# Performance work log

Measured on AMD Instinct MI355X. Metric: run time of the kernel, lower is better.

The kernel has to match this reference:

```python
import jax, jax.numpy as jnp
import numpy as np

B, S, E, H = 2, 2048, 1024, 16
D = E // H  # head_dim = 64
EPS = 1e-6


def _angle_decay():
    # angle: 1/10000**linspace(0,1,D//2), each value repeated twice (interleaved)
    a = 1.0 / (10000.0 ** jnp.linspace(0.0, 1.0, D // 2))
    angle = jnp.repeat(a, 2)  # [D]
    decay = jnp.log(1.0 - 2.0 ** (-5.0 - jnp.arange(H, dtype=jnp.float32)))  # [H]
    return angle, decay


def _rel_pos(slen):
    angle, decay = _angle_decay()
    idx = jnp.arange(slen, dtype=jnp.float32)
    sin = jnp.sin(idx[:, None] * angle[None, :])  # [S, D]
    cos = jnp.cos(idx[:, None] * angle[None, :])  # [S, D]
    diff = idx[:, None] - idx[None, :]            # [S, S]
    tril = diff >= 0
    masked = jnp.where(tril, diff, jnp.inf)
    mask = jnp.exp(masked * decay[:, None, None])  # [H, S, S]; exp(-inf)=0 on upper tri
    mask = jnp.nan_to_num(mask)
    mask = mask / jnp.sqrt(jnp.sum(mask, axis=-1, keepdims=True))
    return sin, cos, mask


def _rotate_every_two(x):
    x1 = x[..., ::2]
    x2 = x[..., 1::2]
    return jnp.stack((-x2, x1), axis=-1).reshape(x.shape)


def _theta_shift(x, sin, cos):
    # x: [B, H, S, D]; sin/cos: [S, D] broadcast over B,H
    return x * cos + _rotate_every_two(x) * sin


def setup_inputs() -> dict:
    key = jax.random.key(0)
    ks = jax.random.split(key, 5)
    scale = 1.0 / np.sqrt(E)
    return {
        "x": jax.random.normal(ks[0], (B, S, E), dtype=jnp.float32),
        "Wq": jax.random.normal(ks[1], (E, E), dtype=jnp.float32) * scale,
        "Wk": jax.random.normal(ks[2], (E, E), dtype=jnp.float32) * scale,
        "Wv": jax.random.normal(ks[3], (E, E), dtype=jnp.float32) * scale,
        "Wg": jax.random.normal(ks[4], (E, E), dtype=jnp.float32) * scale,
    }


def reference(x, Wq, Wk, Wv, Wg):
    bsz, tgt_len, _ = x.shape
    sin, cos, mask = _rel_pos(tgt_len)
    scaling = E ** (-0.5)

    q = x @ Wq
    k = (x @ Wk) * scaling
    v = x @ Wv
    g = x @ Wg

    q = q.reshape(bsz, tgt_len, H, D).transpose(0, 2, 1, 3)  # [B,H,S,D]
    k = k.reshape(bsz, tgt_len, H, D).transpose(0, 2, 1, 3)
    vr = v.reshape(bsz, tgt_len, H, D).transpose(0, 2, 1, 3)

    qr = _theta_shift(q, sin, cos)
    kr = _theta_shift(k, sin, cos)

    qk = jnp.einsum("bhqd,bhkd->bhqk", qr, kr) * mask[None]
    denom = jax.lax.stop_gradient(
        jnp.clip(jnp.sum(jnp.abs(qk), axis=-1, keepdims=True), 1.0, 5e4)
    )
    out = jnp.einsum("bhqk,bhkd->bhqd", qk / denom, vr)
    out = out.transpose(0, 2, 1, 3)  # [B,S,H,D]

    # RMSNorm over head_dim (no affine)
    out = out * jax.lax.rsqrt(jnp.mean(out * out, axis=-1, keepdims=True) + EPS)
    out = out.reshape(bsz, tgt_len, E)
    return jax.nn.silu(g) * out
```

## Files before the change

### kernel.cpp

```cpp
#include <hip/hip_runtime.h>

typedef unsigned short u16;
typedef unsigned int u32;
typedef __attribute__((ext_vector_type(8))) __bf16 bf16x8;
typedef __attribute__((ext_vector_type(4))) float f32x4;

#define B_SZ   2
#define S_LEN  2048
#define E_DIM  1024
#define NHEAD  16
#define HD     64
#define KDIM   1024

__device__ __forceinline__ float bf2f(u16 u){
  union { u32 i; float f; } c; c.i = ((u32)u) << 16; return c.f;
}
__device__ __forceinline__ u16 f2bf(float f){
  union { float f; u32 i; } c; c.f = f;
  return (u16)((c.i + 0x7FFFu + ((c.i >> 16) & 1u)) >> 16);
}
__device__ __forceinline__ u16 f2bf_fast(float f){
  union { float f; u32 i; } c; c.f = f;
  return (u16)((c.i + 0x8000u) >> 16);
}
__device__ __forceinline__ void gl2lds16(const void* g, void* l){
  __builtin_amdgcn_global_load_lds((const __attribute__((address_space(1))) void*)g,
                                   (__attribute__((address_space(3))) void*)l, 16, 0, 0);
}

__global__ __launch_bounds__(256) void prep_kernel(const float* __restrict__ x,
                                                   const float* __restrict__ Wq, const float* __restrict__ Wk,
                                                   const float* __restrict__ Wv, const float* __restrict__ Wg,
                                                   u16* __restrict__ xb, u16* __restrict__ WT){
  __shared__ u16 tile[64][66];
  int z = blockIdx.z;
  int t = threadIdx.x;
  if (z < 4){
    const float* Ws[4] = {Wq, Wk, Wv, Wg};
    const float* W = Ws[z];
    int n0 = blockIdx.x * 64, k0 = blockIdx.y * 64;
    int r = t >> 2, cg = (t & 3) * 16;
    const float* src = W + (size_t)(k0 + r) * E_DIM + n0 + cg;
    float f[16];
    #pragma unroll
    for (int c = 0; c < 4; c++) *(float4*)&f[c * 4] = *(const float4*)&src[c * 4];
    #pragma unroll
    for (int i = 0; i < 16; i++) tile[r][cg + i] = f2bf(f[i]);
    __syncthreads();
    u16 ov[16];
    #pragma unroll
    for (int i = 0; i < 16; i++) ov[i] = tile[cg + i][r];
    int n7 = r & 7, cb = cg >> 3;
    u16* dst = WT + (size_t)(z * E_DIM + n0 + r) * KDIM + k0;
    *(uint4*)&dst[(cb ^ n7) * 8]       = *(uint4*)&ov[0];
    *(uint4*)&dst[((cb + 1) ^ n7) * 8] = *(uint4*)&ov[8];
  } else {
    int blk = (z - 4) * 256 + blockIdx.y * 16 + blockIdx.x;
    size_t flat = ((size_t)blk * 256 + t) * 16;
    int m7 = (int)((flat >> 10) & 7);
    int cb = (int)((flat >> 3) & 7);
    size_t tl = flat & ~(size_t)63;
    float f[16];
    #pragma unroll
    for (int c = 0; c < 4; c++) *(float4*)&f[c * 4] = *(const float4*)&x[flat + c * 4];
    u16 o[16];
    #pragma unroll
    for (int i = 0; i < 16; i++) o[i] = f2bf(f[i]);
    *(uint4*)&xb[tl + ((cb ^ m7) * 8)]       = *(uint4*)&o[0];
    *(uint4*)&xb[tl + (((cb + 1) ^ m7) * 8)] = *(uint4*)&o[8];
  }
}

__global__ __launch_bounds__(512, 2) void gemm_kernel(const u16* __restrict__ A, const u16* __restrict__ Bt,
                                                      u16* __restrict__ qr, u16* __restrict__ kr,
                                                      u16* __restrict__ vt, u16* __restrict__ gc){
  __shared__ __align__(16) u16 SH[65536];
  int m0 = blockIdx.y * 256, n0 = blockIdx.x * 256;
  int t = threadIdx.x;
  int wave = t >> 6, lane = t & 63;
  int l15 = lane & 15, quad = lane >> 4, h8 = lane & 7;
  int wm = wave >> 2, wn = wave & 3;

  f32x4 acc[8][4];
  #pragma unroll
  for (int i = 0; i < 8; i++)
    #pragma unroll
    for (int j = 0; j < 4; j++) acc[i][j] = (f32x4){0.f, 0.f, 0.f, 0.f};

  auto Aoff = [&](int buf, int half) -> int { return (buf * 2 + half) * 8192; };
  auto Boff = [&](int buf, int half) -> int { return 32768 + (buf * 2 + half) * 8192; };

  auto stA = [&](int buf, int half, int kt){
    const u16* src = A + (size_t)(m0 + half * 128) * KDIM + kt * 64;
    #pragma unroll
    for (int c = 0; c < 2; c++){
      int L = c * 512 + t;
      gl2lds16(src + (size_t)(L >> 3) * KDIM + (L & 7) * 8, &SH[Aoff(buf, half) + L * 8]);
    }
  };
  auto stB = [&](int buf, int half, int kt){
    const u16* src = Bt + (size_t)(n0 + half * 128) * KDIM + kt * 64;
    #pragma unroll
    for (int c = 0; c < 2; c++){
      int L = c * 512 + t;
      gl2lds16(src + (size_t)(L >> 3) * KDIM + (L & 7) * 8, &SH[Boff(buf, half) + L * 8]);
    }
  };
  auto ldA = [&](int buf, int i, int ks) -> bf16x8 {
    int r = i * 16 + l15;
    return *(const bf16x8*)&SH[Aoff(buf, wm) + r * 64 + (((ks * 4 + quad) ^ h8) * 8)];
  };
  auto ldB = [&](int buf, int j, int ks) -> bf16x8 {
    int c = (wn & 1) * 64 + j * 16 + l15;
    return *(const bf16x8*)&SH[Boff(buf, wn >> 1) + c * 64 + (((ks * 4 + quad) ^ h8) * 8)];
  };

  stA(0, 0, 0); stB(0, 0, 0); stA(0, 1, 0); stB(0, 1, 0);
  asm volatile("s_waitcnt vmcnt(0)" ::: "memory");
  __builtin_amdgcn_s_barrier();

  bf16x8 a[4][2];
  bf16x8 bA[2][2];
  bf16x8 bB[2][2];

  for (int t2 = 0; t2 < 8; ++t2){
    int kt0 = 2 * t2;
    bool more = (t2 < 7);

    #pragma unroll
    for (int half = 0; half < 2; ++half){
      int buf = half;
      bool stg = (buf == 0) || more;
      {
        #pragma unroll
        for (int i = 0; i < 4; i++){ a[i][0] = ldA(buf, i, 0); a[i][1] = ldA(buf, i, 1); }
        #pragma unroll
        for (int j = 0; j < 2; j++){ bA[j][0] = ldB(buf, j, 0); bA[j][1] = ldB(buf, j, 1); }
        if (buf == 0){ stA(1, 0, kt0 + 1); stB(1, 0, kt0 + 1); }
        else if (more){ stA(0, 0, kt0 + 2); stB(0, 0, kt0 + 2); }
        __builtin_amdgcn_sched_barrier(0);
        __builtin_amdgcn_s_barrier();
        asm volatile("s_waitcnt lgkmcnt(0)" ::: "memory");
        __builtin_amdgcn_sched_barrier(0);
        __builtin_amdgcn_s_setprio(1);
        #pragma unroll
        for (int i = 0; i < 4; i++)
          #pragma unroll
          for (int j = 0; j < 2; j++){
            acc[i][j] = __builtin_amdgcn_mfma_f32_16x16x32_bf16(a[i][0], bA[j][0], acc[i][j], 0, 0, 0);
            acc[i][j] = __builtin_amdgcn_mfma_f32_16x16x32_bf16(a[i][1], bA[j][1], acc[i][j], 0, 0, 0);
          }
        __builtin_amdgcn_s_setprio(0);
        __builtin_amdgcn_sched_barrier(0);
        __builtin_amdgcn_s_barrier();
      }
      {
        #pragma unroll
        for (int j = 0; j < 2; j++){ bB[j][0] = ldB(buf, j + 2, 0); bB[j][1] = ldB(buf, j + 2, 1); }
        if (buf == 0){ stA(1, 1, kt0 + 1); stB(1, 1, kt0 + 1); }
        else if (more){ stA(0, 1, kt0 + 2); stB(0, 1, kt0 + 2); }
        __builtin_amdgcn_sched_barrier(0);
        __builtin_amdgcn_s_barrier();
        asm volatile("s_waitcnt lgkmcnt(0)" ::: "memory");
        __builtin_amdgcn_sched_barrier(0);
        __builtin_amdgcn_s_setprio(1);
        #pragma unroll
        for (int i = 0; i < 4; i++)
          #pragma unroll
          for (int j = 0; j < 2; j++){
            acc[i][j + 2] = __builtin_amdgcn_mfma_f32_16x16x32_bf16(a[i][0], bB[j][0], acc[i][j + 2], 0, 0, 0);
            acc[i][j + 2] = __builtin_amdgcn_mfma_f32_16x16x32_bf16(a[i][1], bB[j][1], acc[i][j + 2], 0, 0, 0);
          }
        __builtin_amdgcn_s_setprio(0);
        __builtin_amdgcn_sched_barrier(0);
        __builtin_amdgcn_s_barrier();
      }
      {
        #pragma unroll
        for (int i = 0; i < 4; i++){ a[i][0] = ldA(buf, i + 4, 0); a[i][1] = ldA(buf, i + 4, 1); }
        __builtin_amdgcn_sched_barrier(0);
        __builtin_amdgcn_s_barrier();
        asm volatile("s_waitcnt lgkmcnt(0)" ::: "memory");
        __builtin_amdgcn_sched_barrier(0);
        __builtin_amdgcn_s_setprio(1);
        #pragma unroll
        for (int i = 0; i < 4; i++)
          #pragma unroll
          for (int j = 0; j < 2; j++){
            acc[i + 4][j + 2] = __builtin_amdgcn_mfma_f32_16x16x32_bf16(a[i][0], bB[j][0], acc[i + 4][j + 2], 0, 0, 0);
            acc[i + 4][j + 2] = __builtin_amdgcn_mfma_f32_16x16x32_bf16(a[i][1], bB[j][1], acc[i + 4][j + 2], 0, 0, 0);
          }
        #pragma unroll
        for (int i = 0; i < 4; i++)
          #pragma unroll
          for (int j = 0; j < 2; j++){
            acc[i + 4][j] = __builtin_amdgcn_mfma_f32_16x16x32_bf16(a[i][0], bA[j][0], acc[i + 4][j], 0, 0, 0);
            acc[i + 4][j] = __builtin_amdgcn_mfma_f32_16x16x32_bf16(a[i][1], bA[j][1], acc[i + 4][j], 0, 0, 0);
          }
        __builtin_amdgcn_s_setprio(0);
        __builtin_amdgcn_sched_barrier(0);
        if (stg) { asm volatile("s_waitcnt vmcnt(0)" ::: "memory"); }
        __builtin_amdgcn_s_barrier();
      }
    }
  }

  __syncthreads();
  u16* epi = SH + wave * 8192;
  int zone = n0 >> 10;
  int n0l = n0 & 1023;
  int hh = (n0l >> 6) + wn;
  int b = m0 >> 11;
  int s0f = (m0 & 2047) + wm * 128;

  if (zone == 2){
    #pragma unroll
    for (int j = 0; j < 4; j++){
      int d = j * 16 + l15;
      #pragma unroll
      for (int i = 0; i < 8; i++){
        int cs0 = i * 2 + (quad >> 1);
        u16 pk[4];
        #pragma unroll
        for (int r = 0; r < 4; r++) pk[r] = f2bf(acc[i][j][r]);
        *(uint2*)&epi[d * 128 + ((cs0 ^ (d & 7)) * 8) + (quad & 1) * 4] = *(uint2*)pk;
      }
    }
    __syncthreads();
    int dl = lane >> 4, cl = lane & 15;
    size_t vbase = (size_t)((b << 4) + hh) * HD * S_LEN;
    #pragma unroll
    for (int it = 0; it < 16; it++){
      int d = it * 4 + dl;
      uint4 v = *(const uint4*)&epi[d * 128 + cl * 8];
      *(uint4*)&vt[vbase + (size_t)d * S_LEN + s0f + cl * 8] = v;
    }
  } else if (zone == 3){
    #pragma unroll
    for (int j = 0; j < 4; j++){
      int c0c = 2 * j + (l15 >> 3), o7 = l15 & 7;
      #pragma unroll
      for (int i = 0; i < 8; i++)
        #pragma unroll
        for (int r = 0; r < 4; r++){
          int row = i * 16 + quad * 4 + r;
          epi[row * 64 + ((c0c ^ (row & 7)) * 8) + o7] = f2bf(acc[i][j][r]);
        }
    }
    __syncthreads();
    int rl = lane >> 3, cl = lane & 7;
    #pragma unroll
    for (int it = 0; it < 16; it++){
      int row = it * 8 + rl;
      uint4 v = *(const uint4*)&epi[row * 64 + ((cl ^ (row & 7)) * 8)];
      *(uint4*)&gc[(size_t)(m0 + wm * 128 + row) * E_DIM + n0l + wn * 64 + cl * 8] = v;
    }
  } else {
    float scale = (zone == 1) ? 0.03125f : 1.0f;
    float sgn = (l15 & 1) ? 1.0f : -1.0f;
    #pragma unroll
    for (int j = 0; j < 4; j++){
      int d = j * 16 + l15;
      int c0c = 2 * j + (l15 >> 3), o7 = l15 & 7;
      float af = exp2f(-(float)(d >> 1) * (13.287712379549449f / 31.0f));
      float cs, sn, ca1, sa1, cb, sb_;
      __sincosf((float)(s0f + quad * 4) * af, &sn, &cs);
      __sincosf(af, &sa1, &ca1);
      __sincosf(13.0f * af, &sb_, &cb);
      #pragma unroll
      for (int i = 0; i < 8; i++)
        #pragma unroll
        for (int r = 0; r < 4; r++){
          int row = i * 16 + quad * 4 + r;
          float vv = acc[i][j][r] * scale;
          float p = __shfl_xor(vv, 1);
          float outv = vv * cs + sgn * p * sn;
          epi[row * 64 + ((c0c ^ (row & 7)) * 8) + o7] = f2bf(outv);
          float nc, ns;
          if (r < 3){ nc = cs * ca1 - sn * sa1; ns = sn * ca1 + cs * sa1; }
          else      { nc = cs * cb  - sn * sb_; ns = sn * cb  + cs * sb_; }
          cs = nc; sn = ns;
        }
    }
    __syncthreads();
    int rl = lane >> 3, cl = lane & 7;
    size_t qkbase = (size_t)((b << 4) + hh) * S_LEN + s0f;
    u16* dst = (zone == 0) ? qr : kr;
    #pragma unroll
    for (int it = 0; it < 16; it++){
      int row = it * 8 + rl;
      int rp = (zone == 0) ? (cl ^ (row & 7)) : cl;
      uint4 v = *(const uint4*)&epi[row * 64 + rp * 8];
      *(uint4*)&dst[(qkbase + row) * HD + cl * 8] = v;
    }
  }
}

__global__ __launch_bounds__(256, 2) void retention_kernel(const u16* __restrict__ qr, const u16* __restrict__ kr,
                                                           const u16* __restrict__ vt,
                                                           u16* __restrict__ pO, u16* __restrict__ pBa){
  int bh = blockIdx.x;
  int qb = 15 - (int)blockIdx.y;
  int z  = blockIdx.z;
  int h = bh & 15;
  int q0 = qb * 128;
  __shared__ __align__(16) u16 Ks[2][64 * 64];
  __shared__ __align__(16) u16 Vs[2][64 * 64];
  __shared__ __align__(16) u16 Ps[128 * 72];
  int t = threadIdx.x, wave = t >> 6, lane = t & 63;
  int l15 = lane & 15, quad = lane >> 4, h8 = lane & 7;

  float decay = log1pf(-exp2f(-5.0f - (float)h));
  float negd = -decay;
  float estep = __expf(64.0f * negd);

  int qsE[2], rowb[2];
  #pragma unroll
  for (int e = 0; e < 2; e++){ rowb[e] = wave * 32 + e * 16; qsE[e] = q0 + rowb[e]; }

  bf16x8 qB[2][2];
  #pragma unroll
  for (int e = 0; e < 2; e++){
    size_t qrow = ((size_t)bh * S_LEN + qsE[e] + l15) * HD;
    qB[e][0] = *(const bf16x8*)&qr[qrow + quad * 8];
    qB[e][1] = *(const bf16x8*)&qr[qrow + 32 + quad * 8];
  }

  float win_f = 11.0f / negd;
  int win_i = (win_f > 2.1e9f) ? 0x7f000000 : (int)win_f;
  int nk = 2 * qb + 2;
  int z_lo = (z * nk) >> 2;
  int z_hi = (((z + 1) * nk) >> 2) - 1;
  int kb_lo = z_lo;
  {
    int jmin = q0 - win_i;
    if (jmin > z_lo * 64){ int wlo = jmin >> 6; kb_lo = wlo > z_lo ? wlo : z_lo; }
  }
  int k0s = kb_lo * 64;

  float em1d = expm1f(decay);
  float rfE[2]; int iE[2];
  #pragma unroll
  for (int e = 0; e < 2; e++){
    int i = qsE[e] + l15;
    iE[e] = i;
    float rowsum = expm1f((float)(i + 1) * decay) / em1d;
    rfE[e] = __expf((float)(i - k0s) * decay) * rsqrtf(rowsum);
  }
  float e1 = __expf(negd);
  float c16 = __expf(negd * 16.0f);
  float cbr[4];
  cbr[0] = __expf(negd * (float)(quad * 4));
  cbr[1] = cbr[0] * e1; cbr[2] = cbr[1] * e1; cbr[3] = cbr[2] * e1;

  f32x4 o[2][4];
  #pragma unroll
  for (int e = 0; e < 2; e++)
    #pragma unroll
    for (int dt = 0; dt < 4; dt++) o[e][dt] = (f32x4){0.f, 0.f, 0.f, 0.f};
  float babs[2] = {0.f, 0.f};

  const u16* krbh = kr + (size_t)bh * S_LEN * HD;
  const u16* vtbh = vt + (size_t)bh * HD * S_LEN;

  if (kb_lo <= z_hi){
    {
      int k0 = kb_lo * 64;
      #pragma unroll
      for (int c = 0; c < 2; c++){
        int L = c * 256 + t;
        gl2lds16(krbh + (size_t)k0 * HD + L * 8, &Ks[0][L * 8]);
      }
      #pragma unroll
      for (int c = 0; c < 2; c++){
        int L = c * 256 + t;
        gl2lds16(vtbh + (size_t)(L >> 3) * S_LEN + k0 + (L & 7) * 8, &Vs[0][L * 8]);
      }
    }
    __syncthreads();
    int cur = 0;
    for (int kb = kb_lo; kb <= z_hi; kb++){
      if (kb < z_hi){
        int k0n = (kb + 1) * 64;
        #pragma unroll
        for (int c = 0; c < 2; c++){
          int L = c * 256 + t;
          gl2lds16(krbh + (size_t)k0n * HD + L * 8, &Ks[cur ^ 1][L * 8]);
        }
        #pragma unroll
        for (int c = 0; c < 2; c++){
          int L = c * 256 + t;
          gl2lds16(vtbh + (size_t)(L >> 3) * S_LEN + k0n + (L & 7) * 8, &Vs[cur ^ 1][L * 8]);
        }
      }
      int k0 = kb * 64;
      const u16* KsC = &Ks[cur][0];
      const u16* VsC = &Vs[cur][0];

      bf16x8 kA0[4], kA1[4];
      #pragma unroll
      for (int ct = 0; ct < 4; ct++){
        int rw = (ct * 16 + l15) * 64;
        kA0[ct] = *(const bf16x8*)&KsC[rw + ((quad ^ h8) * 8)];
        kA1[ct] = *(const bf16x8*)&KsC[rw + (((quad + 4) ^ h8) * 8)];
      }
      #pragma unroll
      for (int e = 0; e < 2; e++){
        int qs = qsE[e];
        if (k0 <= qs + 15 && k0 + 63 >= qs - win_i){
          bool diag = (k0 + 64 > qs);
          float cf[4] = {cbr[0], cbr[1], cbr[2], cbr[3]};
          #pragma unroll
          for (int ct = 0; ct < 4; ct++){
            f32x4 zacc = (f32x4){0.f, 0.f, 0.f, 0.f};
            zacc = __builtin_amdgcn_mfma_f32_16x16x32_bf16(kA0[ct], qB[e][0], zacc, 0, 0, 0);
            zacc = __builtin_amdgcn_mfma_f32_16x16x32_bf16(kA1[ct], qB[e][1], zacc, 0, 0, 0);
            u16 pk[4];
            #pragma unroll
            for (int r = 0; r < 4; r++){
              float p = zacc[r] * (rfE[e] * cf[r]);
              if (diag && (k0 + ct * 16 + quad * 4 + r) > iE[e]) p = 0.f;
              babs[e] += fabsf(p);
              pk[r] = f2bf_fast(p);
              cf[r] *= c16;
            }
            u32 lo = (u32)pk[0] | ((u32)pk[1] << 16);
            u32 hi = (u32)pk[2] | ((u32)pk[3] << 16);
            *(uint2*)&Ps[(rowb[e] + l15) * 72 + ct * 16 + quad * 4] = make_uint2(lo, hi);
          }
        }
      }
      #pragma unroll
      for (int e = 0; e < 2; e++){
        int qs = qsE[e];
        if (k0 <= qs + 15 && k0 + 63 >= qs - win_i){
          bf16x8 pB0 = *(const bf16x8*)&Ps[(rowb[e] + l15) * 72 + quad * 8];
          bf16x8 pB1 = *(const bf16x8*)&Ps[(rowb[e] + l15) * 72 + 32 + quad * 8];
          #pragma unroll
          for (int dt = 0; dt < 4; dt++){
            int rw = (dt * 16 + l15) * 64;
            bf16x8 vA0 = *(const bf16x8*)&VsC[rw + ((quad ^ h8) * 8)];
            bf16x8 vA1 = *(const bf16x8*)&VsC[rw + (((quad + 4) ^ h8) * 8)];
            o[e][dt] = __builtin_amdgcn_mfma_f32_16x16x32_bf16(vA0, pB0, o[e][dt], 0, 0, 0);
            o[e][dt] = __builtin_amdgcn_mfma_f32_16x16x32_bf16(vA1, pB1, o[e][dt], 0, 0, 0);
          }
        }
      }
      #pragma unroll
      for (int e = 0; e < 2; e++) rfE[e] *= estep;
      __syncthreads();
      cur ^= 1;
    }
  }

  size_t slot = ((size_t)bh * 16 + qb) * 4 + z;
  u16* po = pO + slot * (4 * 128 * 16);
  #pragma unroll
  for (int e = 0; e < 2; e++){
    float bsum = babs[e];
    bsum += __shfl_xor(bsum, 16);
    bsum += __shfl_xor(bsum, 32);
    if (quad == 0) pBa[slot * 128 + rowb[e] + l15] = f2bf(bsum);
    #pragma unroll
    for (int dt = 0; dt < 4; dt++){
      u16 pk[4];
      #pragma unroll
      for (int r = 0; r < 4; r++) pk[r] = f2bf(o[e][dt][r]);
      *(uint2*)&po[(dt * 128 + rowb[e] + l15) * 16 + quad * 4] = *(uint2*)pk;
    }
  }
}

__global__ __launch_bounds__(128) void combine_kernel(const u16* __restrict__ pO, const u16* __restrict__ pBa,
                                                      const u16* __restrict__ gc, float* __restrict__ out){
  int bh = blockIdx.x, qb = blockIdx.y;
  int b = bh >> 4, h = bh & 15;
  int i = threadIdx.x;
  int s = qb * 128 + i;
  size_t s4 = ((size_t)bh * 16 + qb) * 4;
  float v[64];
  #pragma unroll
  for (int d = 0; d < 64; d++) v[d] = 0.f;
  float bsum = 0.f;
  #pragma unroll
  for (int z = 0; z < 4; z++){
    const u16* pz = pO + (s4 + z) * 8192;
    #pragma unroll
    for (int dt = 0; dt < 4; dt++){
      u16 a[16];
      *(uint4*)&a[0] = *(const uint4*)&pz[(dt * 128 + i) * 16];
      *(uint4*)&a[8] = *(const uint4*)&pz[(dt * 128 + i) * 16 + 8];
      #pragma unroll
      for (int c = 0; c < 16; c++) v[dt * 16 + c] += bf2f(a[c]);
    }
    bsum += bf2f(pBa[(s4 + z) * 128 + i]);
  }
  float dinv = 1.0f / fminf(fmaxf(bsum, 1.0f), 50000.0f);
  float ssq = 0.f;
  #pragma unroll
  for (int d = 0; d < 64; d++){ v[d] *= dinv; ssq += v[d] * v[d]; }
  float rms = rsqrtf(ssq * (1.0f / 64.0f) + 1e-6f);
  size_t gbase = ((size_t)b * S_LEN + s) * E_DIM + h * HD;
  u16 gu[64];
  #pragma unroll
  for (int c = 0; c < 8; c++) *(uint4*)&gu[c * 8] = *(const uint4*)&gc[gbase + c * 8];
  float ov[64];
  #pragma unroll
  for (int d = 0; d < 64; d++){
    float gv = bf2f(gu[d]);
    float sg = gv / (1.0f + __expf(-gv));
    ov[d] = v[d] * rms * sg;
  }
  float* obase = out + ((size_t)b * S_LEN + s) * E_DIM + h * HD;
  #pragma unroll
  for (int c = 0; c < 16; c++) *(float4*)&obase[c * 4] = *(float4*)&ov[c * 4];
}

extern "C" void kernel_launch(void* const* d_in, const int* in_sizes, int n_in,
                              void* d_out, int out_size, void* d_ws, size_t ws_size,
                              hipStream_t stream){
  const float* x  = (const float*)d_in[0];
  const float* Wq = (const float*)d_in[1];
  const float* Wk = (const float*)d_in[2];
  const float* Wv = (const float*)d_in[3];
  const float* Wg = (const float*)d_in[4];
  float* out = (float*)d_out;
  char* ws = (char*)d_ws;
  u16* xb  = (u16*)(ws);
  u16* WT  = (u16*)(ws + (8ull  << 20));
  u16* pO  = (u16*)(ws);
  u16* qrp = (u16*)(ws + (32ull << 20));
  u16* krp = (u16*)(ws + (40ull << 20));
  u16* vtp = (u16*)(ws + (48ull << 20));
  u16* gcp = (u16*)(ws + (56ull << 20));
  u16* pBa = (u16*)(ws + (64ull << 20));

  prep_kernel     <<<dim3(16, 16, 8),  256, 0, stream>>>(x, Wq, Wk, Wv, Wg, xb, WT);
  gemm_kernel     <<<dim3(16, 16),     512, 0, stream>>>(xb, WT, qrp, krp, vtp, gcp);
  retention_kernel<<<dim3(32, 16, 4),  256, 0, stream>>>(qrp, krp, vtp, pO, pBa);
  combine_kernel  <<<dim3(32, 16),     128, 0, stream>>>(pO, pBa, gcp, out);
}
```

Measured before the change: 176.7 us.

## Triple-buffer K/V LDS staging with prefetch distance two and partial vmcnt waits

Moves the K/V shared-memory pipeline from double to triple buffering. Loads for tile kb+2 are issued while tile kb is computed. The full __syncthreads is replaced by a partial s_waitcnt vmcnt(4) plus a raw s_barrier, so only the older tile's loads must land before continuing, which hides more global latency. The cost is 16KB more LDS per block, which with 2 blocks per CU may lower occupancy. It also depends on the hand-counted vmcnt matching exactly four outstanding loads per stage.

Measured after the change: 181.5 us. +2.7%, slower.

```diff
diff --git a/kernel.cpp b/kernel.cpp
--- a/kernel.cpp
+++ b/kernel.cpp
@@ -304,8 +304,8 @@
   int z  = blockIdx.z;
   int h = bh & 15;
   int q0 = qb * 128;
-  __shared__ __align__(16) u16 Ks[2][64 * 64];
-  __shared__ __align__(16) u16 Vs[2][64 * 64];
+  __shared__ __align__(16) u16 Ks[3][4096];
+  __shared__ __align__(16) u16 Vs[3][4096];
   __shared__ __align__(16) u16 Ps[128 * 72];
   int t = threadIdx.x, wave = t >> 6, lane = t & 63;
   int l15 = lane & 15, quad = lane >> 4, h8 = lane & 7;
@@ -363,36 +363,37 @@
   const u16* krbh = kr + (size_t)bh * S_LEN * HD;
   const u16* vtbh = vt + (size_t)bh * HD * S_LEN;
 
+  auto stKV = [&](int kb, int slot){
+    int k0 = kb * 64;
+    #pragma unroll
+    for (int c = 0; c < 2; c++){
+      int L = c * 256 + t;
+      gl2lds16(krbh + (size_t)k0 * HD + L * 8, &Ks[slot][L * 8]);
+    }
+    #pragma unroll
+    for (int c = 0; c < 2; c++){
+      int L = c * 256 + t;
+      gl2lds16(vtbh + (size_t)(L >> 3) * S_LEN + k0 + (L & 7) * 8, &Vs[slot][L * 8]);
+    }
+  };
+
   if (kb_lo <= z_hi){
-    {
-      int k0 = kb_lo * 64;
-      #pragma unroll
-      for (int c = 0; c < 2; c++){
-        int L = c * 256 + t;
-        gl2lds16(krbh + (size_t)k0 * HD + L * 8, &Ks[0][L * 8]);
-      }
-      #pragma unroll
-      for (int c = 0; c < 2; c++){
-        int L = c * 256 + t;
-        gl2lds16(vtbh + (size_t)(L >> 3) * S_LEN + k0 + (L & 7) * 8, &Vs[0][L * 8]);
-      }
-    }
-    __syncthreads();
+    stKV(kb_lo, 0);
+    if (kb_lo + 1 <= z_hi){
+      stKV(kb_lo + 1, 1);
+      asm volatile("s_waitcnt vmcnt(4)" ::: "memory");
+    } else {
+      asm volatile("s_waitcnt vmcnt(0)" ::: "memory");
+    }
+    __builtin_amdgcn_sched_barrier(0);
+    __builtin_amdgcn_s_barrier();
+    __builtin_amdgcn_sched_barrier(0);
+
     int cur = 0;
     for (int kb = kb_lo; kb <= z_hi; kb++){
-      if (kb < z_hi){
-        int k0n = (kb + 1) * 64;
-        #pragma unroll
-        for (int c = 0; c < 2; c++){
-          int L = c * 256 + t;
-          gl2lds16(krbh + (size_t)k0n * HD + L * 8, &Ks[cur ^ 1][L * 8]);
-        }
-        #pragma unroll
-        for (int c = 0; c < 2; c++){
-          int L = c * 256 + t;
-          gl2lds16(vtbh + (size_t)(L >> 3) * S_LEN + k0n + (L & 7) * 8, &Vs[cur ^ 1][L * 8]);
-        }
-      }
+      bool stg = (kb + 2 <= z_hi);
+      if (stg) stKV(kb + 2, (cur + 2) % 3);
+
       int k0 = kb * 64;
       const u16* KsC = &Ks[cur][0];
       const u16* VsC = &Vs[cur][0];
@@ -448,8 +449,15 @@
       }
       #pragma unroll
       for (int e = 0; e < 2; e++) rfE[e] *= estep;
-      __syncthreads();
-      cur ^= 1;
+
+      if (kb < z_hi){
+        __builtin_amdgcn_sched_barrier(0);
+        if (stg) { asm volatile("s_waitcnt vmcnt(4)" ::: "memory"); }
+        else     { asm volatile("s_waitcnt vmcnt(0)" ::: "memory"); }
+        __builtin_amdgcn_s_barrier();
+        __builtin_amdgcn_sched_barrier(0);
+      }
+      cur = (cur == 2) ? 0 : cur + 1;
     }
   }
 
```
